# Optimization experiments

Hardware: AMD Instinct MI355X
Metric: run time of the kernel (lower is better)

The kernel has to match this reference:

```python
import jax, jax.numpy as jnp
import numpy as np

N_NODES = 100000
N_EDGES = 1600000
IN_DIM, HID_DIM, OUT_DIM = 128, 128, 64


def setup_inputs() -> dict:
    key = jax.random.key(0)
    ks = jax.random.split(key, 5)
    x = jax.random.normal(ks[0], (N_NODES, IN_DIM), dtype=jnp.float32)
    edge_index = jax.random.randint(ks[1], (2, N_EDGES), 0, N_NODES, dtype=jnp.int64)
    W1 = jax.random.normal(ks[2], (IN_DIM, HID_DIM), dtype=jnp.float32) * (1.0 / np.sqrt(IN_DIM))
    b1 = jnp.zeros((HID_DIM,), dtype=jnp.float32)
    W2 = jax.random.normal(ks[3], (HID_DIM, OUT_DIM), dtype=jnp.float32) * (1.0 / np.sqrt(HID_DIM))
    b2 = jnp.zeros((OUT_DIM,), dtype=jnp.float32)
    return {"x": x, "edge_index": edge_index, "W1": W1, "b1": b1, "W2": W2, "b2": b2}


def _gcn_conv(h, row, col, norm, b, n_nodes):
    # h: [N, F] already linearly transformed; message = norm_e * h[src]; scatter-add to dst
    msg = h[row] * norm[:, None]                      # [E+N, F]
    out = jax.ops.segment_sum(msg, col, num_segments=n_nodes)
    return out + b


def reference(x, edge_index, W1, b1, W2, b2):
    n = x.shape[0]
    loops = jnp.arange(n, dtype=edge_index.dtype)
    row = jnp.concatenate([edge_index[0], loops])     # sources (incl. self loops)
    col = jnp.concatenate([edge_index[1], loops])     # targets
    # symmetric normalization: deg over targets with unit edge weights
    deg = jax.ops.segment_sum(jnp.ones_like(col, dtype=x.dtype), col, num_segments=n)
    dinv = jnp.where(deg > 0, jax.lax.rsqrt(jnp.maximum(deg, 1.0)), 0.0)
    norm = dinv[row] * dinv[col]                      # [E+N]
    h = jax.nn.relu(_gcn_conv(x @ W1, row, col, norm, b1, n))
    out = _gcn_conv(h @ W2, row, col, norm, b2, n)
    return out.mean(axis=0)                           # [OUT_DIM]
```

## Files before the change

### kernel.cpp

```cpp
#include <hip/hip_runtime.h>

#define N_NODES 100000
#define N_EDGES 1600000
#define IN_DIM 128
#define HID_DIM 128
#define OUT_DIM 64
#define BKT_SHIFT 7
#define BKT_SIZE 128
#define NBKT ((N_NODES + BKT_SIZE - 1) / BKT_SIZE)
#define B1 256
#define HIST_N (NBKT * B1)
#define HIST_N2 (2 * HIST_N)
#define GEMM_BLKS ((N_NODES + 127) / 128)
#define AGG_BLKS 2048
#define NPW 13

typedef float v2f __attribute__((ext_vector_type(2)));
typedef float v4f __attribute__((ext_vector_type(4)));
typedef short v8s __attribute__((ext_vector_type(8)));

__device__ __forceinline__ int permb(int b) { return ((b & 7) << 5) | (b >> 3); }

__device__ __forceinline__ unsigned int f2bf(float f) {
  unsigned int u = __float_as_uint(f);
  return (u + 0x7FFFu + ((u >> 16) & 1u)) >> 16;
}

template <bool HI>
__device__ __forceinline__ v2f cvt8(unsigned int u) {
  return __builtin_amdgcn_cvt_pk_f32_fp8((int)u, HI);
}

__device__ __forceinline__ float redq(float v) {
  v += __shfl_xor(v, 16);
  v += __shfl_xor(v, 32);
  return v;
}

__device__ __forceinline__ void load4(const void* ei, int is64, int half, int base,
                                      int* v) {
  if (is64) {
    const long long* e = (const long long*)ei + (size_t)half * N_EDGES + base;
    longlong2 a = *(const longlong2*)e;
    longlong2 b = *(const longlong2*)(e + 2);
    v[0] = (int)a.x; v[1] = (int)a.y; v[2] = (int)b.x; v[3] = (int)b.y;
  } else {
    const int* e = (const int*)ei + (size_t)half * N_EDGES + base;
    int4 a = *(const int4*)e;
    v[0] = a.x; v[1] = a.y; v[2] = a.z; v[3] = a.w;
  }
}

__device__ __forceinline__ int detect64_block(const unsigned int* ei, int* sh) {
  if (threadIdx.x == 0) *sh = 0;
  __syncthreads();
  if (ei[1 + 2 * threadIdx.x] != 0u) *sh = 1;
  __syncthreads();
  return (*sh == 0) ? 1 : 0;
}

__global__ __launch_bounds__(256) void front_kernel(const float* __restrict__ x,
                                                    const float* __restrict__ W,
                                                    const void* ei,
                                                    unsigned int* __restrict__ G,
                                                    int* hist, float* S) {
  __shared__ __align__(16) char smem[2 * 128 * 136 * 2];
  if (blockIdx.x >= GEMM_BLKS) {
    int* hd = (int*)smem;
    int* hs = hd + NBKT;
    int* sh = hs + NBKT;
    const int hb = blockIdx.x - GEMM_BLKS;
    const int pj = permb(hb);
    if (hb == 0 && threadIdx.x < HID_DIM) S[threadIdx.x] = 0.f;
    const int is64 = detect64_block((const unsigned int*)ei, sh);
    for (int k = threadIdx.x; k < NBKT; k += 256) { hd[k] = 0; hs[k] = 0; }
    __syncthreads();
    for (int g = hb * 256 + threadIdx.x; g < N_EDGES / 4; g += B1 * 256) {
      int r[4], c[4];
      load4(ei, is64, 0, g * 4, r);
      load4(ei, is64, 1, g * 4, c);
#pragma unroll
      for (int k = 0; k < 4; k++) {
        atomicAdd(&hd[c[k] >> BKT_SHIFT], 1);
        atomicAdd(&hs[r[k] >> BKT_SHIFT], 1);
      }
    }
    __syncthreads();
    for (int k = threadIdx.x; k < NBKT; k += 256) {
      hist[k * B1 + pj] = hd[k];
      hist[HIST_N + k * B1 + pj] = hs[k];
    }
    return;
  }
  typedef unsigned short us_row[136];
  us_row* lx = (us_row*)smem;
  us_row* lwt = (us_row*)(smem + 128 * 136 * 2);
  const int t = threadIdx.x;
  const int row0 = blockIdx.x * 128;

  {
    const float4* W4 = (const float4*)W;
    for (int it = 0; it < 16; ++it) {
      int idx = t + 256 * it;
      int k = idx >> 5, c4 = (idx & 31) * 4;
      float4 w = W4[idx];
      lwt[c4 + 0][k] = (unsigned short)f2bf(w.x);
      lwt[c4 + 1][k] = (unsigned short)f2bf(w.y);
      lwt[c4 + 2][k] = (unsigned short)f2bf(w.z);
      lwt[c4 + 3][k] = (unsigned short)f2bf(w.w);
    }
  }
  {
    const float4* x4 = (const float4*)(x + (size_t)row0 * IN_DIM);
    for (int it = 0; it < 16; ++it) {
      int idx = t + 256 * it;
      int r = idx >> 5, kq = (idx & 31) * 4;
      float4 v = make_float4(0.f, 0.f, 0.f, 0.f);
      if (row0 + r < N_NODES) v = x4[idx];
      unsigned int p0 = (f2bf(v.y) << 16) | f2bf(v.x);
      unsigned int p1 = (f2bf(v.w) << 16) | f2bf(v.z);
      *(uint2*)&lx[r][kq] = make_uint2(p0, p1);
    }
  }
  __syncthreads();

  const int lane = t & 63;
  const int wv = t >> 6;
  const int m0 = wv * 32;
  const int lrow = lane & 15;
  const int lk = (lane >> 4) * 8;

  v4f acc[2][8];
#pragma unroll
  for (int si = 0; si < 2; si++)
#pragma unroll
    for (int n = 0; n < 8; n++) acc[si][n] = (v4f){0.f, 0.f, 0.f, 0.f};

#pragma unroll
  for (int kk = 0; kk < 128; kk += 32) {
    v8s a0 = *(const v8s*)&lx[m0 + lrow][kk + lk];
    v8s a1 = *(const v8s*)&lx[m0 + 16 + lrow][kk + lk];
#pragma unroll
    for (int n = 0; n < 8; n++) {
      v8s b = *(const v8s*)&lwt[n * 16 + lrow][kk + lk];
      acc[0][n] = __builtin_amdgcn_mfma_f32_16x16x32_bf16(a0, b, acc[0][n], 0, 0, 0);
      acc[1][n] = __builtin_amdgcn_mfma_f32_16x16x32_bf16(a1, b, acc[1][n], 0, 0, 0);
    }
  }

  unsigned char* G8 = (unsigned char*)G;
#pragma unroll
  for (int si = 0; si < 2; si++)
#pragma unroll
    for (int n = 0; n < 8; n++) {
      int colg = n * 16 + (lane & 15);
#pragma unroll
      for (int i = 0; i < 4; i++) {
        int r = row0 + m0 + si * 16 + (lane >> 4) * 4 + i;
        if (r < N_NODES) {
          float v = acc[si][n][i];
          int pk = __builtin_amdgcn_cvt_pk_fp8_f32(v, v, 0, false);
          G8[(size_t)r * HID_DIM + colg] = (unsigned char)(pk & 0xFF);
        }
      }
    }
}

__global__ void scan1_kernel(int* arr, int* bsum, int n) {
  __shared__ int tmp[256];
  int i = blockIdx.x * 256 + threadIdx.x;
  int v = (i < n) ? arr[i] : 0;
  tmp[threadIdx.x] = v;
  __syncthreads();
  for (int off = 1; off < 256; off <<= 1) {
    int t2 = (threadIdx.x >= off) ? tmp[threadIdx.x - off] : 0;
    __syncthreads();
    tmp[threadIdx.x] += t2;
    __syncthreads();
  }
  if (i < n) arr[i] = tmp[threadIdx.x] - v;
  if (threadIdx.x == 255) bsum[blockIdx.x] = tmp[255];
}

__global__ void scan2_kernel(int* bsum, int nb) {
  __shared__ int tmp[1024];
  const int t = threadIdx.x;
  int v0 = (2 * t < nb) ? bsum[2 * t] : 0;
  int v1 = (2 * t + 1 < nb) ? bsum[2 * t + 1] : 0;
  int s = v0 + v1;
  tmp[t] = s;
  __syncthreads();
  for (int off = 1; off < 1024; off <<= 1) {
    int t2 = (t >= off) ? tmp[t - off] : 0;
    __syncthreads();
    tmp[t] += t2;
    __syncthreads();
  }
  int excl = tmp[t] - s;
  if (2 * t < nb) bsum[2 * t] = excl;
  if (2 * t + 1 < nb) bsum[2 * t + 1] = excl + v0;
}

__global__ __launch_bounds__(256) void scatter_kernel(const void* ei, const int* hist,
                                                      const int* bsum,
                                                      unsigned int* pairs) {
  __shared__ int cd[NBKT], cs[NBKT], sh[1];
  const int is64 = detect64_block((const unsigned int*)ei, sh);
  const int pj = permb(blockIdx.x);
  for (int k = threadIdx.x; k < NBKT; k += 256) {
    cd[k] = hist[k * B1 + pj] + bsum[k];
    cs[k] = hist[HIST_N + k * B1 + pj] + bsum[NBKT + k];
  }
  __syncthreads();
  for (int g = blockIdx.x * 256 + threadIdx.x; g < N_EDGES / 4; g += B1 * 256) {
    int r[4], c[4];
    load4(ei, is64, 0, g * 4, r);
    load4(ei, is64, 1, g * 4, c);
#pragma unroll
    for (int k = 0; k < 4; k++) {
      int pd = atomicAdd(&cd[c[k] >> BKT_SHIFT], 1);
      pairs[pd] = ((unsigned int)(c[k] & (BKT_SIZE - 1)) << 17) | (unsigned int)r[k];
      int ps = atomicAdd(&cs[r[k] >> BKT_SHIFT], 1);
      pairs[ps] = ((unsigned int)(r[k] & (BKT_SIZE - 1)) << 17) | (unsigned int)c[k];
    }
  }
}

__global__ __launch_bounds__(256) void csrA_kernel(const int* hist, const int* bsum,
                                                   const unsigned int* pairs,
                                                   int* rowptr, float* dinv) {
  __shared__ int cnt[BKT_SIZE], sc[BKT_SIZE];
  const int k = blockIdx.x;
  const int base = hist[k * B1] + bsum[k];
  const int end = (k == NBKT - 1) ? N_EDGES : hist[(k + 1) * B1] + bsum[k + 1];
  const int nseg = end - base;
  const int l = threadIdx.x;
  if (l < BKT_SIZE) cnt[l] = 0;
  __syncthreads();
  for (int i = l; i < nseg; i += 256) atomicAdd(&cnt[pairs[base + i] >> 17], 1);
  __syncthreads();
  if (l < BKT_SIZE) sc[l] = cnt[l];
  __syncthreads();
  for (int off = 1; off < BKT_SIZE; off <<= 1) {
    int v = (l < BKT_SIZE && l >= off) ? sc[l - off] : 0;
    __syncthreads();
    if (l < BKT_SIZE) sc[l] += v;
    __syncthreads();
  }
  if (l < BKT_SIZE) {
    int excl = sc[l] - cnt[l];
    int v = k * BKT_SIZE + l;
    if (v < N_NODES) {
      rowptr[v] = base + excl;
      dinv[v] = rsqrtf((float)(cnt[l] + 1));
    }
  }
  if (k == NBKT - 1 && l == 0) rowptr[N_NODES] = N_EDGES;
}

__global__ __launch_bounds__(256) void csrBout_kernel(const int* hist, const int* bsum,
                                                      const unsigned int* pairs,
                                                      const int* __restrict__ rowptr,
                                                      const float* __restrict__ dinv,
                                                      unsigned int* __restrict__ csr,
                                                      float* __restrict__ wacc) {
  if (blockIdx.x < NBKT) {
    __shared__ int cur[BKT_SIZE];
    const int k = blockIdx.x;
    const int base = hist[k * B1] + bsum[k];
    const int end = (k == NBKT - 1) ? N_EDGES : hist[(k + 1) * B1] + bsum[k + 1];
    const int nseg = end - base;
    const int l = threadIdx.x;
    if (l < BKT_SIZE) {
      int v = k * BKT_SIZE + l;
      cur[l] = (v < N_NODES) ? rowptr[v] : 0;
    }
    __syncthreads();
    int i = l;
    for (; i + 768 < nseg; i += 1024) {
      const unsigned int pk0 = pairs[base + i];
      const unsigned int pk1 = pairs[base + i + 256];
      const unsigned int pk2 = pairs[base + i + 512];
      const unsigned int pk3 = pairs[base + i + 768];
      const unsigned int s0 = pk0 & 0x1FFFFu, s1 = pk1 & 0x1FFFFu;
      const unsigned int s2 = pk2 & 0x1FFFFu, s3 = pk3 & 0x1FFFFu;
      const float d0 = dinv[s0], d1 = dinv[s1], d2 = dinv[s2], d3 = dinv[s3];
      const int p0 = atomicAdd(&cur[pk0 >> 17], 1);
      const int p1 = atomicAdd(&cur[pk1 >> 17], 1);
      const int p2 = atomicAdd(&cur[pk2 >> 17], 1);
      const int p3 = atomicAdd(&cur[pk3 >> 17], 1);
      csr[p0] = (f2bf(d0) << 17) | s0;
      csr[p1] = (f2bf(d1) << 17) | s1;
      csr[p2] = (f2bf(d2) << 17) | s2;
      csr[p3] = (f2bf(d3) << 17) | s3;
    }
    for (; i < nseg; i += 256) {
      const unsigned int pk = pairs[base + i];
      const unsigned int src = pk & 0x1FFFFu;
      const int pos = atomicAdd(&cur[pk >> 17], 1);
      csr[pos] = (f2bf(dinv[src]) << 17) | src;
    }
    return;
  }
  __shared__ float fb[BKT_SIZE];
  const int k = blockIdx.x - NBKT;
  const int base = hist[HIST_N + k * B1] + bsum[NBKT + k];
  const int end =
      (k == NBKT - 1) ? 2 * N_EDGES : hist[HIST_N + (k + 1) * B1] + bsum[NBKT + k + 1];
  if (threadIdx.x < BKT_SIZE) fb[threadIdx.x] = 0.f;
  __syncthreads();
  int i = base + threadIdx.x;
  for (; i + 768 < end; i += 1024) {
    const unsigned int pk0 = pairs[i];
    const unsigned int pk1 = pairs[i + 256];
    const unsigned int pk2 = pairs[i + 512];
    const unsigned int pk3 = pairs[i + 768];
    const float d0 = dinv[pk0 & 0x1FFFFu];
    const float d1 = dinv[pk1 & 0x1FFFFu];
    const float d2 = dinv[pk2 & 0x1FFFFu];
    const float d3 = dinv[pk3 & 0x1FFFFu];
    atomicAdd(&fb[pk0 >> 17], d0);
    atomicAdd(&fb[pk1 >> 17], d1);
    atomicAdd(&fb[pk2 >> 17], d2);
    atomicAdd(&fb[pk3 >> 17], d3);
  }
  for (; i < end; i += 256) {
    const unsigned int pk = pairs[i];
    atomicAdd(&fb[pk >> 17], dinv[pk & 0x1FFFFu]);
  }
  __syncthreads();
  int v = k * BKT_SIZE + threadIdx.x;
  if (threadIdx.x < BKT_SIZE && v < N_NODES) wacc[v] = fb[threadIdx.x];
}

__global__ __launch_bounds__(256) void aggregate_kernel(
    const unsigned int* __restrict__ G, const int* __restrict__ rowptr,
    const unsigned int* __restrict__ csr, const float* __restrict__ dinv,
    const float* __restrict__ wacc, const float* __restrict__ b1,
    float* __restrict__ S) {
  __shared__ float lb[HID_DIM];
  __shared__ float ls[HID_DIM];
  if (threadIdx.x < HID_DIM) {
    lb[threadIdx.x] = b1[threadIdx.x];
    ls[threadIdx.x] = 0.f;
  }
  __syncthreads();

  const int lane = threadIdx.x & 63;
  const int q = lane >> 4;
  const int r = lane & 15;
  const int wid = blockIdx.x * 4 + (threadIdx.x >> 6);
  const int c0 = wid * NPW;
  const uint2* __restrict__ G2 = (const uint2*)G;

  int rp = 0;
  float dvv = 0.f, wvv = 0.f;
  {
    const int ci = c0 + lane;
    if (lane <= NPW && ci <= N_NODES) rp = rowptr[ci];
    if (lane < NPW && ci < N_NODES) { dvv = dinv[ci]; wvv = wacc[ci]; }
  }

  v2f s01 = {0.f, 0.f}, s23 = {0.f, 0.f}, s45 = {0.f, 0.f}, s67 = {0.f, 0.f};
  const int nn = (c0 < N_NODES) ? min(NPW, N_NODES - c0) : 0;

  if (nn > 0) {
    int kF = 0, jF = 0;
    const int sF0 = __shfl(rp, 0);
    int cnumF = __shfl(rp, 1) - sF0;
    int SF = max(1, (cnumF + 15) >> 4);
    unsigned int pwW = 0;
    if (lane < cnumF) pwW = __builtin_nontemporal_load(&csr[sF0 + lane]);
    int sN = __shfl(rp, 1);
    int eN = __shfl(rp, 2);
    unsigned int pwN = 0;
    if (1 < nn && sN + lane < eN) pwN = __builtin_nontemporal_load(&csr[sN + lane]);

    int kC = 0, jC = 0;
    int SC = SF;
    float dC = __shfl(dvv, 0), waC = __shfl(wvv, 0);
    v2f a01 = {0.f, 0.f}, a23 = {0.f, 0.f}, a45 = {0.f, 0.f}, a67 = {0.f, 0.f};

    uint2 gA[4], gB[4], gSA, gSB;
    unsigned int wpA[2], wpB[2];

    auto FETCH = [&](uint2(&g)[4], unsigned int(&wp)[2], uint2& gS) {
      if (jF != 0 && (jF & 3) == 0) {
        const int sAbs = __shfl(rp, kF) + (jF << 4);
        pwW = 0;
        if ((jF << 4) + lane < cnumF)
          pwW = __builtin_nontemporal_load(&csr[sAbs + lane]);
      }
      const int base = (jF & 3) << 4;
      const int eg0 = (jF << 4) + q;
      unsigned int wb[4];
#pragma unroll
      for (int t = 0; t < 4; ++t) {
        const unsigned int p = __shfl(pwW, base + 4 * t + q);
        const bool vld = eg0 + 4 * t < cnumF;
        wb[t] = vld ? ((p >> 17) << 16) : 0u;
        g[t] = make_uint2(0u, 0u);
        if (vld) g[t] = G2[(size_t)(p & 0x1FFFFu) * 16 + r];
      }
      wp[0] = wb[0] | (wb[1] >> 16);
      wp[1] = wb[2] | (wb[3] >> 16);
      if (jF == 0) {
        gS = make_uint2(0u, 0u);
        if (q == 0) gS = G2[(size_t)(c0 + kF) * 16 + r];
      }
      if (jF + 1 < SF) { jF++; return; }
      kF++; jF = 0;
      if (kF < nn) {
        pwW = pwN;
        cnumF = eN - sN;
        SF = max(1, (cnumF + 15) >> 4);
        if (kF + 1 < nn) {
          sN = __shfl(rp, kF + 1);
          eN = __shfl(rp, kF + 2);
          pwN = 0;
          if (sN + lane < eN) pwN = __builtin_nontemporal_load(&csr[sN + lane]);
        }
      }
    };

    auto CONSUME = [&](const uint2(&g)[4], const unsigned int(&wp)[2],
                       const uint2& gS) -> bool {
      const float w0 = __uint_as_float(wp[0] & 0xFFFF0000u);
      const float w1 = __uint_as_float(wp[0] << 16);
      const float w2 = __uint_as_float(wp[1] & 0xFFFF0000u);
      const float w3 = __uint_as_float(wp[1] << 16);
      a01 += cvt8<false>(g[0].x) * w0; a23 += cvt8<true>(g[0].x) * w0;
      a45 += cvt8<false>(g[0].y) * w0; a67 += cvt8<true>(g[0].y) * w0;
      a01 += cvt8<false>(g[1].x) * w1; a23 += cvt8<true>(g[1].x) * w1;
      a45 += cvt8<false>(g[1].y) * w1; a67 += cvt8<true>(g[1].y) * w1;
      a01 += cvt8<false>(g[2].x) * w2; a23 += cvt8<true>(g[2].x) * w2;
      a45 += cvt8<false>(g[2].y) * w2; a67 += cvt8<true>(g[2].y) * w2;
      a01 += cvt8<false>(g[3].x) * w3; a23 += cvt8<true>(g[3].x) * w3;
      a45 += cvt8<false>(g[3].y) * w3; a67 += cvt8<true>(g[3].y) * w3;
      if (jC == 0 && q == 0) {
        a01 += cvt8<false>(gS.x) * dC; a23 += cvt8<true>(gS.x) * dC;
        a45 += cvt8<false>(gS.y) * dC; a67 += cvt8<true>(gS.y) * dC;
      }
      if (jC + 1 < SC) { jC++; return true; }
      const float A0 = redq(a01.x), A1 = redq(a01.y);
      const float A2 = redq(a23.x), A3 = redq(a23.y);
      const float A4 = redq(a45.x), A5 = redq(a45.y);
      const float A6 = redq(a67.x), A7 = redq(a67.y);
      if (q == 0) {
        const float wc = dC * (waC + dC);
        const float* bb = &lb[8 * r];
        s01.x += wc * fmaxf(fmaf(dC, A0, bb[0]), 0.f);
        s01.y += wc * fmaxf(fmaf(dC, A1, bb[1]), 0.f);
        s23.x += wc * fmaxf(fmaf(dC, A2, bb[2]), 0.f);
        s23.y += wc * fmaxf(fmaf(dC, A3, bb[3]), 0.f);
        s45.x += wc * fmaxf(fmaf(dC, A4, bb[4]), 0.f);
        s45.y += wc * fmaxf(fmaf(dC, A5, bb[5]), 0.f);
        s67.x += wc * fmaxf(fmaf(dC, A6, bb[6]), 0.f);
        s67.y += wc * fmaxf(fmaf(dC, A7, bb[7]), 0.f);
      }
      a01 = (v2f){0.f, 0.f}; a23 = (v2f){0.f, 0.f};
      a45 = (v2f){0.f, 0.f}; a67 = (v2f){0.f, 0.f};
      kC++; jC = 0;
      if (kC >= nn) return false;
      const int s_ = __shfl(rp, kC);
      const int cnumC = __shfl(rp, kC + 1) - s_;
      SC = max(1, (cnumC + 15) >> 4);
      dC = __shfl(dvv, kC);
      waC = __shfl(wvv, kC);
      return true;
    };

    FETCH(gA, wpA, gSA);
    for (;;) {
      if (kF < nn) FETCH(gB, wpB, gSB);
      if (!CONSUME(gA, wpA, gSA)) break;
      if (kF < nn) FETCH(gA, wpA, gSA);
      if (!CONSUME(gB, wpB, gSB)) break;
    }
  }

  if (q == 0) {
    atomicAdd(&ls[8 * r + 0], s01.x); atomicAdd(&ls[8 * r + 1], s01.y);
    atomicAdd(&ls[8 * r + 2], s23.x); atomicAdd(&ls[8 * r + 3], s23.y);
    atomicAdd(&ls[8 * r + 4], s45.x); atomicAdd(&ls[8 * r + 5], s45.y);
    atomicAdd(&ls[8 * r + 6], s67.x); atomicAdd(&ls[8 * r + 7], s67.y);
  }
  __syncthreads();
  if (threadIdx.x < HID_DIM) atomicAdd(&S[threadIdx.x], ls[threadIdx.x]);
}

__global__ void finish_kernel(const float* __restrict__ S, const float* __restrict__ W2,
                              const float* __restrict__ b2, float* __restrict__ out) {
  int j = threadIdx.x;
  float acc = 0.f;
  for (int k = 0; k < HID_DIM; k++) acc += S[k] * W2[k * OUT_DIM + j];
  out[j] = acc * (1.0f / N_NODES) + b2[j];
}

extern "C" void kernel_launch(void* const* d_in, const int* in_sizes, int n_in,
                              void* d_out, int out_size, void* d_ws, size_t ws_size,
                              hipStream_t stream) {
  const float* x  = (const float*)d_in[0];
  const void*  ei = d_in[1];
  const float* W1 = (const float*)d_in[2];
  const float* b1 = (const float*)d_in[3];
  const float* W2 = (const float*)d_in[4];
  const float* b2 = (const float*)d_in[5];
  float* out = (float*)d_out;

  char* p = (char*)d_ws;
  size_t off = 0;
  auto alloc = [&](size_t bytes) -> void* {
    void* r = p + off;
    off = (off + bytes + 63) & ~(size_t)63;
    return r;
  };
  int*   hist   = (int*)alloc((size_t)HIST_N2 * 4);
  int*   bsum   = (int*)alloc(2048 * 4);
  unsigned int* pairs = (unsigned int*)alloc((size_t)2 * N_EDGES * 4);
  int*   rowptr = (int*)alloc(((size_t)N_NODES + 1) * 4);
  unsigned int* csr = (unsigned int*)alloc((size_t)N_EDGES * 4);
  float* dinv   = (float*)alloc((size_t)N_NODES * 4);
  float* wacc   = (float*)alloc((size_t)N_NODES * 4);
  float* S      = (float*)alloc(HID_DIM * 4);
  unsigned int* G = (unsigned int*)alloc((size_t)N_NODES * HID_DIM);
  (void)ws_size; (void)n_in; (void)in_sizes; (void)out_size;

  const int NBH = HIST_N2 / 256;

  front_kernel<<<GEMM_BLKS + B1, 256, 0, stream>>>(x, W1, ei, G, hist, S);
  scan1_kernel<<<NBH, 256, 0, stream>>>(hist, bsum, HIST_N2);
  scan2_kernel<<<1, 1024, 0, stream>>>(bsum, NBH);
  scatter_kernel<<<B1, 256, 0, stream>>>(ei, hist, bsum, pairs);
  csrA_kernel<<<NBKT, 256, 0, stream>>>(hist, bsum, pairs, rowptr, dinv);
  csrBout_kernel<<<2 * NBKT, 256, 0, stream>>>(hist, bsum, pairs, rowptr, dinv, csr,
                                               wacc);
  aggregate_kernel<<<AGG_BLKS, 256, 0, stream>>>(G, rowptr, csr, dinv, wacc, b1, S);
  finish_kernel<<<1, 64, 0, stream>>>(S, W2, b2, out);
}
```

Before: 264.9 us.

## Compute node degrees with global atomics in front kernel and drop csrA pass

Adds per-node in-degree counting via global atomics during the histogram pass, computes dinv in extra scan1 blocks, and folds the rowptr prefix scan into the CSR build kernel, removing the separate csrA kernel and its full re-read of the pairs array. In exchange it adds a memset and 1.6M global atomics on random addresses in the front kernel, which may contend.

New measurement: 315.3 us. 1.19x slower.

```diff
diff --git a/kernel.cpp b/kernel.cpp
--- a/kernel.cpp
+++ b/kernel.cpp
@@ -11,7 +11,9 @@
 #define B1 256
 #define HIST_N (NBKT * B1)
 #define HIST_N2 (2 * HIST_N)
+#define NBH2 (HIST_N2 / 256)
 #define GEMM_BLKS ((N_NODES + 127) / 128)
+#define NODE_BLKS ((N_NODES + 255) / 256)
 #define AGG_BLKS 2048
 #define NPW 13
 
@@ -63,7 +65,8 @@
                                                     const float* __restrict__ W,
                                                     const void* ei,
                                                     unsigned int* __restrict__ G,
-                                                    int* hist, float* S) {
+                                                    int* hist, float* S,
+                                                    int* __restrict__ deg) {
   __shared__ __align__(16) char smem[2 * 128 * 136 * 2];
   if (blockIdx.x >= GEMM_BLKS) {
     int* hd = (int*)smem;
@@ -83,6 +86,7 @@
       for (int k = 0; k < 4; k++) {
         atomicAdd(&hd[c[k] >> BKT_SHIFT], 1);
         atomicAdd(&hs[r[k] >> BKT_SHIFT], 1);
+        atomicAdd(&deg[c[k]], 1);
       }
     }
     __syncthreads();
@@ -166,10 +170,16 @@
     }
 }
 
-__global__ void scan1_kernel(int* arr, int* bsum, int n) {
+__global__ void scan1_kernel(int* arr, int* bsum, const int* __restrict__ deg,
+                             float* __restrict__ dinv) {
+  if (blockIdx.x >= NBH2) {
+    const int v = (blockIdx.x - NBH2) * 256 + threadIdx.x;
+    if (v < N_NODES) dinv[v] = rsqrtf((float)(deg[v] + 1));
+    return;
+  }
   __shared__ int tmp[256];
   int i = blockIdx.x * 256 + threadIdx.x;
-  int v = (i < n) ? arr[i] : 0;
+  int v = (i < HIST_N2) ? arr[i] : 0;
   tmp[threadIdx.x] = v;
   __syncthreads();
   for (int off = 1; off < 256; off <<= 1) {
@@ -178,7 +188,7 @@
     tmp[threadIdx.x] += t2;
     __syncthreads();
   }
-  if (i < n) arr[i] = tmp[threadIdx.x] - v;
+  if (i < HIST_N2) arr[i] = tmp[threadIdx.x] - v;
   if (threadIdx.x == 255) bsum[blockIdx.x] = tmp[255];
 }
 
@@ -226,56 +236,40 @@
   }
 }
 
-__global__ __launch_bounds__(256) void csrA_kernel(const int* hist, const int* bsum,
-                                                   const unsigned int* pairs,
-                                                   int* rowptr, float* dinv) {
-  __shared__ int cnt[BKT_SIZE], sc[BKT_SIZE];
-  const int k = blockIdx.x;
-  const int base = hist[k * B1] + bsum[k];
-  const int end = (k == NBKT - 1) ? N_EDGES : hist[(k + 1) * B1] + bsum[k + 1];
-  const int nseg = end - base;
-  const int l = threadIdx.x;
-  if (l < BKT_SIZE) cnt[l] = 0;
-  __syncthreads();
-  for (int i = l; i < nseg; i += 256) atomicAdd(&cnt[pairs[base + i] >> 17], 1);
-  __syncthreads();
-  if (l < BKT_SIZE) sc[l] = cnt[l];
-  __syncthreads();
-  for (int off = 1; off < BKT_SIZE; off <<= 1) {
-    int v = (l < BKT_SIZE && l >= off) ? sc[l - off] : 0;
-    __syncthreads();
-    if (l < BKT_SIZE) sc[l] += v;
-    __syncthreads();
-  }
-  if (l < BKT_SIZE) {
-    int excl = sc[l] - cnt[l];
-    int v = k * BKT_SIZE + l;
-    if (v < N_NODES) {
-      rowptr[v] = base + excl;
-      dinv[v] = rsqrtf((float)(cnt[l] + 1));
-    }
-  }
-  if (k == NBKT - 1 && l == 0) rowptr[N_NODES] = N_EDGES;
-}
-
-__global__ __launch_bounds__(256) void csrBout_kernel(const int* hist, const int* bsum,
-                                                      const unsigned int* pairs,
-                                                      const int* __restrict__ rowptr,
-                                                      const float* __restrict__ dinv,
-                                                      unsigned int* __restrict__ csr,
-                                                      float* __restrict__ wacc) {
+__global__ __launch_bounds__(256) void csrABout_kernel(
+    const int* hist, const int* bsum, const unsigned int* pairs,
+    const int* __restrict__ deg, const float* __restrict__ dinv,
+    int* __restrict__ rowptr, unsigned int* __restrict__ csr,
+    float* __restrict__ wacc) {
   if (blockIdx.x < NBKT) {
-    __shared__ int cur[BKT_SIZE];
+    __shared__ int cur[BKT_SIZE], sc[BKT_SIZE];
+    __shared__ int tot;
     const int k = blockIdx.x;
     const int base = hist[k * B1] + bsum[k];
-    const int end = (k == NBKT - 1) ? N_EDGES : hist[(k + 1) * B1] + bsum[k + 1];
-    const int nseg = end - base;
     const int l = threadIdx.x;
+    int dv = 0;
     if (l < BKT_SIZE) {
       int v = k * BKT_SIZE + l;
-      cur[l] = (v < N_NODES) ? rowptr[v] : 0;
-    }
-    __syncthreads();
+      dv = (v < N_NODES) ? deg[v] : 0;
+      sc[l] = dv;
+    }
+    __syncthreads();
+    for (int off = 1; off < BKT_SIZE; off <<= 1) {
+      int t2 = (l < BKT_SIZE && l >= off) ? sc[l - off] : 0;
+      __syncthreads();
+      if (l < BKT_SIZE) sc[l] += t2;
+      __syncthreads();
+    }
+    if (l < BKT_SIZE) {
+      const int rp = base + sc[l] - dv;
+      const int v = k * BKT_SIZE + l;
+      if (v < N_NODES) rowptr[v] = rp;
+      cur[l] = rp;
+      if (l == BKT_SIZE - 1) tot = sc[l];
+    }
+    if (k == NBKT - 1 && l == 0) rowptr[N_NODES] = N_EDGES;
+    __syncthreads();
+    const int nseg = tot;
     int i = l;
     for (; i + 768 < nseg; i += 1024) {
       const unsigned int pk0 = pairs[base + i];
@@ -515,6 +509,7 @@
     off = (off + bytes + 63) & ~(size_t)63;
     return r;
   };
+  int*   deg    = (int*)alloc((size_t)N_NODES * 4);
   int*   hist   = (int*)alloc((size_t)HIST_N2 * 4);
   int*   bsum   = (int*)alloc(2048 * 4);
   unsigned int* pairs = (unsigned int*)alloc((size_t)2 * N_EDGES * 4);
@@ -526,15 +521,14 @@
   unsigned int* G = (unsigned int*)alloc((size_t)N_NODES * HID_DIM);
   (void)ws_size; (void)n_in; (void)in_sizes; (void)out_size;
 
-  const int NBH = HIST_N2 / 256;
-
-  front_kernel<<<GEMM_BLKS + B1, 256, 0, stream>>>(x, W1, ei, G, hist, S);
-  scan1_kernel<<<NBH, 256, 0, stream>>>(hist, bsum, HIST_N2);
-  scan2_kernel<<<1, 1024, 0, stream>>>(bsum, NBH);
+  hipMemsetAsync(deg, 0, (size_t)N_NODES * 4, stream);
+
+  front_kernel<<<GEMM_BLKS + B1, 256, 0, stream>>>(x, W1, ei, G, hist, S, deg);
+  scan1_kernel<<<NBH2 + NODE_BLKS, 256, 0, stream>>>(hist, bsum, deg, dinv);
+  scan2_kernel<<<1, 1024, 0, stream>>>(bsum, NBH2);
   scatter_kernel<<<B1, 256, 0, stream>>>(ei, hist, bsum, pairs);
-  csrA_kernel<<<NBKT, 256, 0, stream>>>(hist, bsum, pairs, rowptr, dinv);
-  csrBout_kernel<<<2 * NBKT, 256, 0, stream>>>(hist, bsum, pairs, rowptr, dinv, csr,
-                                               wacc);
+  csrABout_kernel<<<2 * NBKT, 256, 0, stream>>>(hist, bsum, pairs, deg, dinv, rowptr,
+                                                csr, wacc);
   aggregate_kernel<<<AGG_BLKS, 256, 0, stream>>>(G, rowptr, csr, dinv, wacc, b1, S);
   finish_kernel<<<1, 64, 0, stream>>>(S, W2, b2, out);
 }
```

## Load x straight into MFMA registers and pack FP8 output in wide stores

Applied to the files above, without the earlier changes.

The GEMM front kernel now loads x rows from global memory straight into per-lane bf16 MFMA operand registers and no longer stages them through LDS, which halves shared memory per block and drops one LDS round trip. The FP8 output is packed four values per word and written as uint2 stores, replacing per-byte stores. This changes the column layout of G so that each lane's 8 columns are strided by 16, and the aggregation kernel's bias and partial-sum indexing is updated to match. The direct global loads are less coalesced per lane, and consistency depends on the hidden gather code agreeing with the new column permutation.

New measurement: 258.1 us (median of 2 runs). -2.5%, faster.

```diff
diff --git a/kernel.cpp b/kernel.cpp
--- a/kernel.cpp
+++ b/kernel.cpp
@@ -64,7 +64,7 @@
                                                     const void* ei,
                                                     unsigned int* __restrict__ G,
                                                     int* hist, float* S) {
-  __shared__ __align__(16) char smem[2 * 128 * 136 * 2];
+  __shared__ __align__(16) char smem[128 * 136 * 2];
   if (blockIdx.x >= GEMM_BLKS) {
     int* hd = (int*)smem;
     int* hs = hd + NBKT;
@@ -93,10 +93,42 @@
     return;
   }
   typedef unsigned short us_row[136];
-  us_row* lx = (us_row*)smem;
-  us_row* lwt = (us_row*)(smem + 128 * 136 * 2);
+  us_row* lwt = (us_row*)smem;
   const int t = threadIdx.x;
   const int row0 = blockIdx.x * 128;
+
+  const int lane = t & 63;
+  const int wv = t >> 6;
+  const int m0 = wv * 32;
+  const int lrow = lane & 15;
+  const int lk = (lane >> 4) * 8;
+
+  v8s a0r[4], a1r[4];
+  {
+    const int r0 = row0 + m0 + lrow;
+    const int r1 = r0 + 16;
+    const float* x0 = x + (size_t)r0 * IN_DIM + lk;
+    const float* x1 = x + (size_t)r1 * IN_DIM + lk;
+    const bool ok0 = r0 < N_NODES, ok1 = r1 < N_NODES;
+    const float4 z4 = make_float4(0.f, 0.f, 0.f, 0.f);
+#pragma unroll
+    for (int kq = 0; kq < 4; ++kq) {
+      float4 fa = z4, fb = z4, fc = z4, fd = z4;
+      if (ok0) { fa = *(const float4*)(x0 + kq * 32); fb = *(const float4*)(x0 + kq * 32 + 4); }
+      if (ok1) { fc = *(const float4*)(x1 + kq * 32); fd = *(const float4*)(x1 + kq * 32 + 4); }
+      v8s p, q;
+      p[0] = (short)f2bf(fa.x); p[1] = (short)f2bf(fa.y);
+      p[2] = (short)f2bf(fa.z); p[3] = (short)f2bf(fa.w);
+      p[4] = (short)f2bf(fb.x); p[5] = (short)f2bf(fb.y);
+      p[6] = (short)f2bf(fb.z); p[7] = (short)f2bf(fb.w);
+      q[0] = (short)f2bf(fc.x); q[1] = (short)f2bf(fc.y);
+      q[2] = (short)f2bf(fc.z); q[3] = (short)f2bf(fc.w);
+      q[4] = (short)f2bf(fd.x); q[5] = (short)f2bf(fd.y);
+      q[6] = (short)f2bf(fd.z); q[7] = (short)f2bf(fd.w);
+      a0r[kq] = p;
+      a1r[kq] = q;
+    }
+  }
 
   {
     const float4* W4 = (const float4*)W;
@@ -110,25 +142,7 @@
       lwt[c4 + 3][k] = (unsigned short)f2bf(w.w);
     }
   }
-  {
-    const float4* x4 = (const float4*)(x + (size_t)row0 * IN_DIM);
-    for (int it = 0; it < 16; ++it) {
-      int idx = t + 256 * it;
-      int r = idx >> 5, kq = (idx & 31) * 4;
-      float4 v = make_float4(0.f, 0.f, 0.f, 0.f);
-      if (row0 + r < N_NODES) v = x4[idx];
-      unsigned int p0 = (f2bf(v.y) << 16) | f2bf(v.x);
-      unsigned int p1 = (f2bf(v.w) << 16) | f2bf(v.z);
-      *(uint2*)&lx[r][kq] = make_uint2(p0, p1);
-    }
-  }
-  __syncthreads();
-
-  const int lane = t & 63;
-  const int wv = t >> 6;
-  const int m0 = wv * 32;
-  const int lrow = lane & 15;
-  const int lk = (lane >> 4) * 8;
+  __syncthreads();
 
   v4f acc[2][8];
 #pragma unroll
@@ -137,9 +151,10 @@
     for (int n = 0; n < 8; n++) acc[si][n] = (v4f){0.f, 0.f, 0.f, 0.f};
 
 #pragma unroll
-  for (int kk = 0; kk < 128; kk += 32) {
-    v8s a0 = *(const v8s*)&lx[m0 + lrow][kk + lk];
-    v8s a1 = *(const v8s*)&lx[m0 + 16 + lrow][kk + lk];
+  for (int kq = 0; kq < 4; ++kq) {
+    const int kk = kq * 32;
+    const v8s a0 = a0r[kq];
+    const v8s a1 = a1r[kq];
 #pragma unroll
     for (int n = 0; n < 8; n++) {
       v8s b = *(const v8s*)&lwt[n * 16 + lrow][kk + lk];
@@ -148,20 +163,18 @@
     }
   }
 
-  unsigned char* G8 = (unsigned char*)G;
+  uint2* Gv = (uint2*)G;
 #pragma unroll
   for (int si = 0; si < 2; si++)
 #pragma unroll
-    for (int n = 0; n < 8; n++) {
-      int colg = n * 16 + (lane & 15);
-#pragma unroll
-      for (int i = 0; i < 4; i++) {
-        int r = row0 + m0 + si * 16 + (lane >> 4) * 4 + i;
-        if (r < N_NODES) {
-          float v = acc[si][n][i];
-          int pk = __builtin_amdgcn_cvt_pk_fp8_f32(v, v, 0, false);
-          G8[(size_t)r * HID_DIM + colg] = (unsigned char)(pk & 0xFF);
-        }
+    for (int i = 0; i < 4; i++) {
+      const int rr = row0 + m0 + si * 16 + (lane >> 4) * 4 + i;
+      if (rr < N_NODES) {
+        int w0 = __builtin_amdgcn_cvt_pk_fp8_f32(acc[si][0][i], acc[si][1][i], 0, false);
+        w0 = __builtin_amdgcn_cvt_pk_fp8_f32(acc[si][2][i], acc[si][3][i], w0, true);
+        int w1 = __builtin_amdgcn_cvt_pk_fp8_f32(acc[si][4][i], acc[si][5][i], 0, false);
+        w1 = __builtin_amdgcn_cvt_pk_fp8_f32(acc[si][6][i], acc[si][7][i], w1, true);
+        Gv[(size_t)rr * 16 + lrow] = make_uint2((unsigned)w0, (unsigned)w1);
       }
     }
 }
@@ -448,15 +461,14 @@
       const float A6 = redq(a67.x), A7 = redq(a67.y);
       if (q == 0) {
         const float wc = dC * (waC + dC);
-        const float* bb = &lb[8 * r];
-        s01.x += wc * fmaxf(fmaf(dC, A0, bb[0]), 0.f);
-        s01.y += wc * fmaxf(fmaf(dC, A1, bb[1]), 0.f);
-        s23.x += wc * fmaxf(fmaf(dC, A2, bb[2]), 0.f);
-        s23.y += wc * fmaxf(fmaf(dC, A3, bb[3]), 0.f);
-        s45.x += wc * fmaxf(fmaf(dC, A4, bb[4]), 0.f);
-        s45.y += wc * fmaxf(fmaf(dC, A5, bb[5]), 0.f);
-        s67.x += wc * fmaxf(fmaf(dC, A6, bb[6]), 0.f);
-        s67.y += wc * fmaxf(fmaf(dC, A7, bb[7]), 0.f);
+        s01.x += wc * fmaxf(fmaf(dC, A0, lb[r]), 0.f);
+        s01.y += wc * fmaxf(fmaf(dC, A1, lb[r + 16]), 0.f);
+        s23.x += wc * fmaxf(fmaf(dC, A2, lb[r + 32]), 0.f);
+        s23.y += wc * fmaxf(fmaf(dC, A3, lb[r + 48]), 0.f);
+        s45.x += wc * fmaxf(fmaf(dC, A4, lb[r + 64]), 0.f);
+        s45.y += wc * fmaxf(fmaf(dC, A5, lb[r + 80]), 0.f);
+        s67.x += wc * fmaxf(fmaf(dC, A6, lb[r + 96]), 0.f);
+        s67.y += wc * fmaxf(fmaf(dC, A7, lb[r + 112]), 0.f);
       }
       a01 = (v2f){0.f, 0.f}; a23 = (v2f){0.f, 0.f};
       a45 = (v2f){0.f, 0.f}; a67 = (v2f){0.f, 0.f};
@@ -480,10 +492,10 @@
   }
 
   if (q == 0) {
-    atomicAdd(&ls[8 * r + 0], s01.x); atomicAdd(&ls[8 * r + 1], s01.y);
-    atomicAdd(&ls[8 * r + 2], s23.x); atomicAdd(&ls[8 * r + 3], s23.y);
-    atomicAdd(&ls[8 * r + 4], s45.x); atomicAdd(&ls[8 * r + 5], s45.y);
-    atomicAdd(&ls[8 * r + 6], s67.x); atomicAdd(&ls[8 * r + 7], s67.y);
+    atomicAdd(&ls[r], s01.x);       atomicAdd(&ls[r + 16], s01.y);
+    atomicAdd(&ls[r + 32], s23.x);  atomicAdd(&ls[r + 48], s23.y);
+    atomicAdd(&ls[r + 64], s45.x);  atomicAdd(&ls[r + 80], s45.y);
+    atomicAdd(&ls[r + 96], s67.x);  atomicAdd(&ls[r + 112], s67.y);
   }
   __syncthreads();
   if (threadIdx.x < HID_DIM) atomicAdd(&S[threadIdx.x], ls[threadIdx.x]);
```
